# Optimization experiments

Measured on AMD Instinct MI355X. Metric: run time of the kernel, lower is better.

Reference implementation:

```python
import jax, jax.numpy as jnp
import numpy as np

H = 512  # hidden_size


def setup_inputs() -> dict:
    key = jax.random.key(0)
    ks = jax.random.split(key, 8)
    B, L = 16, 2048
    query = jax.random.normal(ks[0], (B, 1, 2 * H), dtype=jnp.float32)
    keys = jax.random.normal(ks[1], (B, L, 2 * H), dtype=jnp.float32)
    coverage = jax.random.uniform(ks[2], (B, L, 1), dtype=jnp.float32)
    # alignment MLP: Linear(4H+1 -> 2H, bias) -> tanh -> Linear(2H -> 1, no bias) -> softmax(dim=1)
    s1 = 1.0 / np.sqrt(4 * H + 1)
    W1 = jax.random.uniform(ks[3], (4 * H + 1, 2 * H), jnp.float32, -s1, s1)
    b1 = jax.random.uniform(ks[4], (2 * H,), jnp.float32, -s1, s1)
    s2 = 1.0 / np.sqrt(2 * H)
    W2 = jax.random.uniform(ks[5], (2 * H, 1), jnp.float32, -s2, s2)
    # reduce: Linear(2H -> H, no bias)
    Wr = jax.random.uniform(ks[6], (2 * H, H), jnp.float32, -s2, s2)
    return {"query": query, "keys": keys, "coverage": coverage,
            "W1": W1, "b1": b1, "W2": W2, "Wr": Wr}


def reference(query, keys, coverage, W1, b1, W2, Wr):
    B, L, _ = keys.shape
    q = jnp.broadcast_to(query, (B, L, query.shape[-1]))          # (B,L,2H)
    feat = jnp.concatenate([q, keys, coverage], axis=-1)          # (B,L,4H+1)
    h = jnp.tanh(feat @ W1 + b1)                                  # (B,L,2H)
    scores = h @ W2                                               # (B,L,1)
    attention = jax.nn.softmax(scores, axis=1)                    # softmax over length
    reduced = keys @ Wr                                           # (B,L,H)
    context = jnp.einsum('blo,blh->boh', attention, reduced)      # (B,1,H)
    return context, attention
```

## Files before the change

### kernel.cpp

```cpp
#include <hip/hip_runtime.h>
#include <hip/hip_bf16.h>
#include <stdint.h>

typedef short bf16x8 __attribute__((ext_vector_type(8)));
typedef float f32x4 __attribute__((ext_vector_type(4)));
typedef unsigned int u32x2 __attribute__((ext_vector_type(2)));

__device__ __forceinline__ uint32_t pack2f(float lo, float hi) {
  union { __hip_bfloat162 h; uint32_t u; } c;
  c.h.x = __float2bfloat16(lo);
  c.h.y = __float2bfloat16(hi);
  return c.u;
}

__device__ __forceinline__ unsigned short f32_to_bf16(float f) {
  union { __hip_bfloat16 h; unsigned short u; } c;
  c.h = __float2bfloat16(f);
  return c.u;
}

__device__ __forceinline__ float bfbits_to_f32(uint32_t hi16) {
  union { uint32_t u; float f; } c;
  c.u = hi16 << 16;
  return c.f;
}

__device__ __forceinline__ float fast_tanh(float x) {
  float e = __builtin_amdgcn_exp2f(x * 2.8853900817779268f);
  return 1.0f - 2.0f * __builtin_amdgcn_rcpf(e + 1.0f);
}

#define GLD16(g, l)                                                                    \
  __builtin_amdgcn_global_load_lds((const __attribute__((address_space(1))) void*)(g), \
                                   (__attribute__((address_space(3))) void*)(l), 16, 0, 0)

#define MFMA16(a, b, c) __builtin_amdgcn_mfma_f32_16x16x32_bf16(a, b, c, 0, 0, 0)
#define SBAR0() __builtin_amdgcn_sched_barrier(0)

__global__ void prep_kernel(const float* __restrict__ keys, unsigned short* __restrict__ keysbf,
                            const float* __restrict__ W1, unsigned short* __restrict__ W1kt,
                            const float* __restrict__ query, const float* __restrict__ b1,
                            float* __restrict__ qterm) {
  __shared__ __align__(16) unsigned char smem[16896];
  const int bid = blockIdx.x;
  const int t = threadIdx.x;
  if (bid < 256) {
    float (*tt)[65] = (float(*)[65])smem;
    const int kb = (bid & 15) * 64;
    const int jb = (bid >> 4) * 64;
    const int c = t & 63;
    const int r = t >> 6;
#pragma unroll
    for (int i = 0; i < 16; ++i) {
      const int k = i * 4 + r;
      tt[k][c] = W1[(size_t)(1024 + kb + k) * 1024 + (jb + c)];
    }
    __syncthreads();
#pragma unroll
    for (int i = 0; i < 16; ++i) {
      const int j = i * 4 + r;
      W1kt[(size_t)(jb + j) * 1024 + (kb + c)] = f32_to_bf16(tt[c][j]);
    }
  } else if (bid < 512) {
    float (*part)[64] = (float(*)[64])smem;
    const int q = bid - 256;
    const int b = q >> 4;
    const int j = (q & 15) * 64 + (t & 63);
    const int kq = t >> 6;
    const float* qp = query + b * 1024 + kq * 256;
    const float* wp = W1 + (size_t)(kq * 256) * 1024 + j;
    float acc = 0.f;
#pragma unroll 8
    for (int k = 0; k < 256; ++k) acc += qp[k] * wp[(size_t)k * 1024];
    part[kq][t & 63] = acc;
    __syncthreads();
    if (t < 64) {
      const int jj = (q & 15) * 64 + t;
      qterm[b * 1024 + jj] = b1[jj] + part[0][t] + part[1][t] + part[2][t] + part[3][t];
    }
  } else {
    const size_t base = (size_t)(bid - 512) * 16384;
#pragma unroll
    for (int bt = 0; bt < 2; ++bt) {
      f32x4 v[8];
#pragma unroll
      for (int i = 0; i < 8; ++i)
        v[i] = *(const f32x4*)(keys + base + bt * 8192 + i * 1024 + t * 4);
#pragma unroll
      for (int i = 0; i < 8; ++i) {
        u32x2 p;
        p.x = pack2f(v[i].x, v[i].y);
        p.y = pack2f(v[i].z, v[i].w);
        *(u32x2*)(keysbf + base + bt * 8192 + i * 1024 + t * 4) = p;
      }
    }
  }
}


#define V14_STAGE(kt_, P)                       \
  GLD16(gk0 + (kt_) * 32, (P) + ldst);          \
  GLD16(gw0 + (kt_) * 32, (P) + 16384 + ldst);  \
  GLD16(gk1 + (kt_) * 32, (P) + 8192 + ldst);   \
  GLD16(gw1 + (kt_) * 32, (P) + 24576 + ldst);

#define V14_COMPUTE(P)                                                     \
  {                                                                        \
    bf16x8 af[8], bfv[4];                                                  \
    _Pragma("unroll") for (int mf = 0; mf < 8; ++mf)                       \
        af[mf] = *(const bf16x8*)((P) + abase + mf * 1024);                \
    _Pragma("unroll") for (int nf = 0; nf < 4; ++nf)                       \
        bfv[nf] = *(const bf16x8*)((P) + bbase + nf * 1024);               \
    __builtin_amdgcn_s_setprio(1);                                         \
    _Pragma("unroll") for (int nf = 0; nf < 4; ++nf)                       \
        _Pragma("unroll") for (int mf = 0; mf < 8; ++mf) acc[mf][nf] =     \
            MFMA16(af[mf], bfv[nf], acc[mf][nf]);                          \
    __builtin_amdgcn_s_setprio(0);                                         \
  }

#define V14_ITER(ts_, Pc, Ps)                       \
  asm volatile("s_waitcnt vmcnt(4)" ::: "memory");  \
  __builtin_amdgcn_s_barrier();                     \
  SBAR0();                                          \
  V14_STAGE(ts_, Ps);                               \
  V14_COMPUTE(Pc);

#define V14_TRIPLE(k0, k1, k2)  \
  V14_ITER(k0, P0, P2);         \
  V14_ITER(k1, P1, P0);         \
  V14_ITER(k2, P2, P1);

__global__ __launch_bounds__(512, 2) void gemm_score_v14(
    const unsigned short* __restrict__ keysbf, const unsigned short* __restrict__ W1kt,
    const float* __restrict__ qterm, const float* __restrict__ coverage,
    const float* __restrict__ W1, const float* __restrict__ W2,
    float* __restrict__ scores_part) {
  __shared__ __align__(16) unsigned char lds[102400];
  unsigned char* P0 = lds;
  unsigned char* P1 = lds + 32768;
  unsigned char* P2 = lds + 65536;
  float* Sred = (float*)(lds + 98304);

  const int tid = threadIdx.x;
  const int bid = blockIdx.x;
  const int xcd = bid & 7;
  const int idx = bid >> 3;
  const int rowt = xcd * 16 + (idx >> 2);
  const int colgrp = idx & 3;
  const int row0 = rowt * 256;
  const int col0 = colgrp * 256;
  const int b = row0 >> 11;
  const int w = tid >> 6;
  const int wm = w >> 2, wn = w & 3;
  const int lane = tid & 63;
  const int c16 = lane & 15, q4 = lane >> 4;

  const int swzc = (q4 ^ ((c16 >> 1) & 3)) << 4;
  const int abase = (wm * 128 + c16) * 64 + swzc;
  const int bbase = 16384 + (wn * 64 + c16) * 64 + swzc;

  const int u = (lane & 3) ^ ((lane >> 3) & 3);
  const int r0s = w * 16 + (lane >> 2);
  const unsigned short* gk0 = keysbf + (size_t)(row0 + r0s) * 1024 + u * 8;
  const unsigned short* gk1 = keysbf + (size_t)(row0 + 128 + r0s) * 1024 + u * 8;
  const unsigned short* gw0 = W1kt + (size_t)(col0 + r0s) * 1024 + u * 8;
  const unsigned short* gw1 = W1kt + (size_t)(col0 + 128 + r0s) * 1024 + u * 8;
  const int ldst = w * 1024 + lane * 16;

  f32x4 acc[8][4];
  const f32x4 zz = {0.f, 0.f, 0.f, 0.f};
#pragma unroll
  for (int mf = 0; mf < 8; ++mf)
#pragma unroll
    for (int nf = 0; nf < 4; ++nf) acc[mf][nf] = zz;

  V14_STAGE(0, P0);
  V14_STAGE(1, P1);

  V14_TRIPLE(2, 3, 4)
  V14_TRIPLE(5, 6, 7)
  V14_TRIPLE(8, 9, 10)
  V14_TRIPLE(11, 12, 13)
  V14_TRIPLE(14, 15, 16)
  V14_TRIPLE(17, 18, 19)
  V14_TRIPLE(20, 21, 22)
  V14_TRIPLE(23, 24, 25)
  V14_TRIPLE(26, 27, 28)
  V14_TRIPLE(29, 30, 31)

  asm volatile("s_waitcnt vmcnt(4)" ::: "memory");
  __builtin_amdgcn_s_barrier();
  SBAR0();
  V14_COMPUTE(P0);
  asm volatile("s_waitcnt vmcnt(0)" ::: "memory");
  __builtin_amdgcn_s_barrier();
  SBAR0();
  V14_COMPUTE(P1);

  float covv[8][4];
#pragma unroll
  for (int mf = 0; mf < 8; ++mf)
#pragma unroll
    for (int r = 0; r < 4; ++r)
      covv[mf][r] = coverage[row0 + wm * 128 + mf * 16 + q4 * 4 + r];

  float p_part[8][4];
#pragma unroll
  for (int mf = 0; mf < 8; ++mf)
#pragma unroll
    for (int r = 0; r < 4; ++r) p_part[mf][r] = 0.f;

#pragma unroll
  for (int nf = 0; nf < 4; ++nf) {
    const int col = col0 + wn * 64 + nf * 16 + c16;
    const float qt = qterm[b * 1024 + col];
    const float w1c = W1[(size_t)2048 * 1024 + col];
    const float w2 = W2[col];
#pragma unroll
    for (int mf = 0; mf < 8; ++mf)
#pragma unroll
      for (int r = 0; r < 4; ++r) {
        float v = acc[mf][nf][r] + qt + covv[mf][r] * w1c;
        p_part[mf][r] += fast_tanh(v) * w2;
      }
  }

#pragma unroll
  for (int mf = 0; mf < 8; ++mf)
#pragma unroll
    for (int r = 0; r < 4; ++r) {
      float p = p_part[mf][r];
      p += __shfl_xor(p, 1);
      p += __shfl_xor(p, 2);
      p += __shfl_xor(p, 4);
      p += __shfl_xor(p, 8);
      if (c16 == 0) Sred[w * 128 + mf * 16 + q4 * 4 + r] = p;
    }
  __syncthreads();
  if (tid < 256) {
    const int wmv = tid >> 7, rl = tid & 127;
    float s = Sred[(wmv * 4 + 0) * 128 + rl] + Sred[(wmv * 4 + 1) * 128 + rl] +
              Sred[(wmv * 4 + 2) * 128 + rl] + Sred[(wmv * 4 + 3) * 128 + rl];
    scores_part[(size_t)colgrp * 32768 + row0 + tid] = s;
  }
}

__global__ void softmax_kernel(const float* __restrict__ sp, float* __restrict__ att) {
  const int b = blockIdx.x;
  const int tid = threadIdx.x;
  float* a = att + b * 2048;
  __shared__ float red[4];
  float mx = -1e30f;
  for (int l = tid; l < 2048; l += 256) {
    float v = 0.f;
#pragma unroll
    for (int g = 0; g < 4; ++g) v += sp[(size_t)g * 32768 + b * 2048 + l];
    a[l] = v;
    mx = fmaxf(mx, v);
  }
#pragma unroll
  for (int o = 1; o < 64; o <<= 1) mx = fmaxf(mx, __shfl_xor(mx, o));
  if ((tid & 63) == 0) red[tid >> 6] = mx;
  __syncthreads();
  mx = fmaxf(fmaxf(red[0], red[1]), fmaxf(red[2], red[3]));
  __syncthreads();
  float sum = 0.f;
  for (int l = tid; l < 2048; l += 256) {
    float e = __expf(a[l] - mx);
    a[l] = e;
    sum += e;
  }
#pragma unroll
  for (int o = 1; o < 64; o <<= 1) sum += __shfl_xor(sum, o);
  if ((tid & 63) == 0) red[tid >> 6] = sum;
  __syncthreads();
  sum = red[0] + red[1] + red[2] + red[3];
  const float inv = 1.0f / sum;
  for (int l = tid; l < 2048; l += 256) a[l] *= inv;
}

__global__ void ctxpre_kernel(const unsigned short* __restrict__ keysbf,
                              const float* __restrict__ att, float* __restrict__ ctx_part) {
  const int b = blockIdx.x;
  const int sl = blockIdx.y;
  const int tid = threadIdx.x;
  const float* ab = att + b * 2048 + sl * 128;
  const unsigned short* kb = keysbf + ((size_t)b * 2048 + sl * 128) * 1024 + tid * 4;
  f32x4 acc = {0.f, 0.f, 0.f, 0.f};
#pragma unroll 4
  for (int l = 0; l < 128; ++l) {
    u32x2 v = *(const u32x2*)(kb + (size_t)l * 1024);
    const float al = ab[l];
    acc.x += bfbits_to_f32(v.x & 0xFFFFu) * al;
    acc.y += bfbits_to_f32(v.x >> 16) * al;
    acc.z += bfbits_to_f32(v.y & 0xFFFFu) * al;
    acc.w += bfbits_to_f32(v.y >> 16) * al;
  }
  *(f32x4*)(ctx_part + ((size_t)(sl * 16 + b)) * 1024 + tid * 4) = acc;
}

__global__ void ctx2_kernel(const float* __restrict__ ctx_part, const float* __restrict__ Wr,
                            float* __restrict__ out) {
  __shared__ float cpre[1024];
  __shared__ float part[4][64];
  const int hb = blockIdx.x;
  const int b = blockIdx.y;
  const int t = threadIdx.x;
#pragma unroll
  for (int jj = 0; jj < 4; ++jj) {
    const int j = jj * 256 + t;
    float s = 0.f;
#pragma unroll
    for (int sl = 0; sl < 16; ++sl) s += ctx_part[((size_t)(sl * 16 + b)) * 1024 + j];
    cpre[j] = s;
  }
  __syncthreads();
  const int h = hb * 64 + (t & 63);
  const int jq = t >> 6;
  const float* wp = Wr + (size_t)(jq * 256) * 512 + h;
  float acc = 0.f;
#pragma unroll 8
  for (int k = 0; k < 256; ++k) acc += cpre[jq * 256 + k] * wp[(size_t)k * 512];
  part[jq][t & 63] = acc;
  __syncthreads();
  if (t < 64)
    out[b * 512 + hb * 64 + t] = part[0][t] + part[1][t] + part[2][t] + part[3][t];
}

extern "C" void kernel_launch(void* const* d_in, const int* in_sizes, int n_in, void* d_out,
                              int out_size, void* d_ws, size_t ws_size, hipStream_t stream) {
  const float* query = (const float*)d_in[0];
  const float* keys = (const float*)d_in[1];
  const float* coverage = (const float*)d_in[2];
  const float* W1 = (const float*)d_in[3];
  const float* b1 = (const float*)d_in[4];
  const float* W2 = (const float*)d_in[5];
  const float* Wr = (const float*)d_in[6];
  float* out = (float*)d_out;
  char* ws = (char*)d_ws;

  float* scores_part = (float*)ws;
  float* ctx_part = (float*)ws;
  float* qterm = (float*)(ws + 1114112);
  unsigned short* W1kt = (unsigned short*)(ws + 1179648);
  unsigned short* keysbf = (unsigned short*)(ws + 3276800);

  float* context_out = out;
  float* att_out = out + 8192;

  prep_kernel<<<dim3(2560), dim3(256), 0, stream>>>(keys, keysbf, W1, W1kt, query, b1, qterm);
  gemm_score_v14<<<dim3(512), dim3(512), 0, stream>>>(keysbf, W1kt, qterm, coverage, W1, W2,
                                                      scores_part);
  softmax_kernel<<<dim3(16), dim3(256), 0, stream>>>(scores_part, att_out);
  ctxpre_kernel<<<dim3(16, 16), dim3(256), 0, stream>>>(keysbf, att_out, ctx_part);
  ctx2_kernel<<<dim3(8, 16), dim3(256), 0, stream>>>(ctx_part, Wr, context_out);
}
```

Before: 140.1 us.

## Switch GEMM mainloop to double-buffered LDS with split-half interleaved prefetch

Replaces the triple-buffered LDS pipeline (prefetch depth 2, vmcnt(4)) with a double buffer. Each K-step is split into two halves, and the global-to-LDS loads for the next tile are issued between the halves' MFMA blocks. This cuts LDS from 100KB to 68KB per block, which may allow more resident blocks. In exchange, every iteration now waits on vmcnt(0) with only one tile of lookahead, which can expose global memory latency and adds extra barriers.

New measurement: 143.4 us. +2.3%, slower.

```diff
diff --git a/kernel.cpp b/kernel.cpp
--- a/kernel.cpp
+++ b/kernel.cpp
@@ -98,48 +98,55 @@
 }
 
 
-#define V14_STAGE(kt_, P)                       \
-  GLD16(gk0 + (kt_) * 32, (P) + ldst);          \
-  GLD16(gw0 + (kt_) * 32, (P) + 16384 + ldst);  \
-  GLD16(gk1 + (kt_) * 32, (P) + 8192 + ldst);   \
-  GLD16(gw1 + (kt_) * 32, (P) + 24576 + ldst);
-
-#define V14_COMPUTE(P)                                                     \
+#define V15_ITER(kt_, Pc, Ps, LAST)                                        \
+  asm volatile("s_waitcnt vmcnt(0) lgkmcnt(0)" ::: "memory");              \
+  __builtin_amdgcn_s_barrier();                                            \
+  SBAR0();                                                                 \
   {                                                                        \
     bf16x8 af[8], bfv[4];                                                  \
-    _Pragma("unroll") for (int mf = 0; mf < 8; ++mf)                       \
-        af[mf] = *(const bf16x8*)((P) + abase + mf * 1024);                \
+    _Pragma("unroll") for (int mf = 0; mf < 4; ++mf)                       \
+        af[mf] = *(const bf16x8*)((Pc) + abase + mf * 1024);               \
     _Pragma("unroll") for (int nf = 0; nf < 4; ++nf)                       \
-        bfv[nf] = *(const bf16x8*)((P) + bbase + nf * 1024);               \
+        bfv[nf] = *(const bf16x8*)((Pc) + bbase + nf * 1024);              \
+    if (!(LAST)) {                                                         \
+      GLD16(gk0 + ((kt_) + 1) * 32, (Ps) + ldst);                          \
+      GLD16(gw0 + ((kt_) + 1) * 32, (Ps) + 16384 + ldst);                  \
+    }                                                                      \
+    SBAR0();                                                               \
     __builtin_amdgcn_s_setprio(1);                                         \
     _Pragma("unroll") for (int nf = 0; nf < 4; ++nf)                       \
-        _Pragma("unroll") for (int mf = 0; mf < 8; ++mf) acc[mf][nf] =     \
-            MFMA16(af[mf], bfv[nf], acc[mf][nf]);                          \
+        _Pragma("unroll") for (int mf = 0; mf < 4; ++mf)                   \
+            acc[mf][nf] = MFMA16(af[mf], bfv[nf], acc[mf][nf]);            \
     __builtin_amdgcn_s_setprio(0);                                         \
-  }
-
-#define V14_ITER(ts_, Pc, Ps)                       \
-  asm volatile("s_waitcnt vmcnt(4)" ::: "memory");  \
-  __builtin_amdgcn_s_barrier();                     \
-  SBAR0();                                          \
-  V14_STAGE(ts_, Ps);                               \
-  V14_COMPUTE(Pc);
-
-#define V14_TRIPLE(k0, k1, k2)  \
-  V14_ITER(k0, P0, P2);         \
-  V14_ITER(k1, P1, P0);         \
-  V14_ITER(k2, P2, P1);
-
-__global__ __launch_bounds__(512, 2) void gemm_score_v14(
+    SBAR0();                                                               \
+    __builtin_amdgcn_s_barrier();                                          \
+    _Pragma("unroll") for (int mf = 4; mf < 8; ++mf)                       \
+        af[mf] = *(const bf16x8*)((Pc) + abase + mf * 1024);               \
+    if (!(LAST)) {                                                         \
+      GLD16(gk1 + ((kt_) + 1) * 32, (Ps) + 8192 + ldst);                   \
+      GLD16(gw1 + ((kt_) + 1) * 32, (Ps) + 24576 + ldst);                  \
+    }                                                                      \
+    SBAR0();                                                               \
+    __builtin_amdgcn_s_setprio(1);                                         \
+    _Pragma("unroll") for (int nf = 0; nf < 4; ++nf)                       \
+        _Pragma("unroll") for (int mf = 4; mf < 8; ++mf)                   \
+            acc[mf][nf] = MFMA16(af[mf], bfv[nf], acc[mf][nf]);            \
+    __builtin_amdgcn_s_setprio(0);                                         \
+  }
+
+#define V15_PAIR(k0, k1) \
+  V15_ITER(k0, P0, P1, false) \
+  V15_ITER(k1, P1, P0, false)
+
+__global__ __launch_bounds__(512, 2) void gemm_score_v15(
     const unsigned short* __restrict__ keysbf, const unsigned short* __restrict__ W1kt,
     const float* __restrict__ qterm, const float* __restrict__ coverage,
     const float* __restrict__ W1, const float* __restrict__ W2,
     float* __restrict__ scores_part) {
-  __shared__ __align__(16) unsigned char lds[102400];
+  __shared__ __align__(16) unsigned char lds[69632];
   unsigned char* P0 = lds;
   unsigned char* P1 = lds + 32768;
-  unsigned char* P2 = lds + 65536;
-  float* Sred = (float*)(lds + 98304);
+  float* Sred = (float*)(lds + 65536);
 
   const int tid = threadIdx.x;
   const int bid = blockIdx.x;
@@ -174,28 +181,28 @@
 #pragma unroll
     for (int nf = 0; nf < 4; ++nf) acc[mf][nf] = zz;
 
-  V14_STAGE(0, P0);
-  V14_STAGE(1, P1);
-
-  V14_TRIPLE(2, 3, 4)
-  V14_TRIPLE(5, 6, 7)
-  V14_TRIPLE(8, 9, 10)
-  V14_TRIPLE(11, 12, 13)
-  V14_TRIPLE(14, 15, 16)
-  V14_TRIPLE(17, 18, 19)
-  V14_TRIPLE(20, 21, 22)
-  V14_TRIPLE(23, 24, 25)
-  V14_TRIPLE(26, 27, 28)
-  V14_TRIPLE(29, 30, 31)
-
-  asm volatile("s_waitcnt vmcnt(4)" ::: "memory");
-  __builtin_amdgcn_s_barrier();
-  SBAR0();
-  V14_COMPUTE(P0);
-  asm volatile("s_waitcnt vmcnt(0)" ::: "memory");
-  __builtin_amdgcn_s_barrier();
-  SBAR0();
-  V14_COMPUTE(P1);
+  GLD16(gk0, P0 + ldst);
+  GLD16(gw0, P0 + 16384 + ldst);
+  GLD16(gk1, P0 + 8192 + ldst);
+  GLD16(gw1, P0 + 24576 + ldst);
+
+  V15_PAIR(0, 1)
+  V15_PAIR(2, 3)
+  V15_PAIR(4, 5)
+  V15_PAIR(6, 7)
+  V15_PAIR(8, 9)
+  V15_PAIR(10, 11)
+  V15_PAIR(12, 13)
+  V15_PAIR(14, 15)
+  V15_PAIR(16, 17)
+  V15_PAIR(18, 19)
+  V15_PAIR(20, 21)
+  V15_PAIR(22, 23)
+  V15_PAIR(24, 25)
+  V15_PAIR(26, 27)
+  V15_PAIR(28, 29)
+  V15_ITER(30, P0, P1, false)
+  V15_ITER(31, P1, P0, true)
 
   float covv[8][4];
 #pragma unroll
@@ -349,7 +356,7 @@
   float* att_out = out + 8192;
 
   prep_kernel<<<dim3(2560), dim3(256), 0, stream>>>(keys, keysbf, W1, W1kt, query, b1, qterm);
-  gemm_score_v14<<<dim3(512), dim3(512), 0, stream>>>(keysbf, W1kt, qterm, coverage, W1, W2,
+  gemm_score_v15<<<dim3(512), dim3(512), 0, stream>>>(keysbf, W1kt, qterm, coverage, W1, W2,
                                                       scores_part);
   softmax_kernel<<<dim3(16), dim3(256), 0, stream>>>(scores_part, att_out);
   ctxpre_kernel<<<dim3(16, 16), dim3(256), 0, stream>>>(keysbf, att_out, ctx_part);
```
